# Optimization experiments

Measured on AMD Instinct MI355X. Metric: run time of the kernel, lower is better.

Reference implementation:

```python
import jax, jax.numpy as jnp
import numpy as np
import math

D = 256   # d_model / hidden_size
Q = 256   # q_num (query-side nodes)
K = 512   # k_num (key-side nodes)
NEG = -9e15


def _forward(q_enc, k_enc, rel_k, rel_v, k_adj,
             W_glob, b_glob, W_gv0, b_gv0, W_gv1, b_gv1,
             W_gq, b_gq, W_lq, b_lq,
             W_locgate, b_locgate, W_gate, b_gate):
    d = q_enc.shape[-1]
    scale = 1.0 / math.sqrt(d)
    act = jnp.tanh  # activation_func='tanh'

    # --- global sigmoid blending of k_enc with the mean query encoding ---
    q_glob_enc = jnp.mean(q_enc, axis=0)                       # [d]
    k_s = jax.nn.sigmoid((q_glob_enc @ W_glob + b_glob) @ k_enc.T * scale)  # [K]
    k_s = k_s[:, None]                                         # [K,1]
    g_1 = q_glob_enc @ W_gv0 + b_gv0                           # [d]
    k_1 = k_enc @ W_gv1 + b_gv1                                # [K,d]
    k_enc2 = (1.0 - k_s) * k_1 + k_s * g_1                     # [K,d]

    # --- global relation-aware attention over k nodes ---
    q_glob = q_enc @ W_gq + b_gq                               # [Q,d]
    qk_logit = q_glob @ k_enc2.T                               # [Q,K]
    qk_r = jnp.einsum('qd,qkd->qk', q_glob, rel_k)             # [Q,K]
    glob_attn = jax.nn.softmax(act((qk_logit + qk_r) * scale), axis=-1)  # [Q,K]

    # --- local adjacency-masked attention ---
    q_loc = q_enc @ W_lq + b_lq                                # [Q,d]
    qnk_logit = q_loc @ k_enc2.T                               # [Q,K]
    qnk_r = jnp.einsum('qd,qkd->qk', q_loc, rel_k)             # [Q,K]
    loc_attn = act((qnk_logit + qnk_r) * scale)                # [Q,K]
    # loc_weight_rep[q,i,j] = loc_attn[q,j]  (repeat + view in torch)
    mask = (k_adj != 0)[None, :, :]                            # [1,K,K]
    masked = jnp.where(mask, loc_attn[:, None, :], NEG)        # [Q,K,K]
    attn_adj_norm = jax.nn.softmax(masked, axis=-1)            # [Q,K,K]
    k_loc = jnp.einsum('qij,jd->qid', attn_adj_norm, k_enc2)   # [Q,K,d]

    # --- local gate between neighborhood value and self value ---
    # sigmoid(cat([k_loc, k_self]) @ W_locgate + b); k_self is broadcast k_enc2
    Wg1, Wg2 = W_locgate[:d], W_locgate[d:]                    # [d,1] each
    gate_logit = (jnp.einsum('qid,d->qi', k_loc, Wg1[:, 0])
                  + (k_enc2 @ Wg2)[None, :, 0] + b_locgate[0])  # [Q,K]
    loc_gate = jax.nn.sigmoid(gate_logit)[..., None]           # [Q,K,1]
    k_awr = loc_gate * k_loc + (1.0 - loc_gate) * k_enc2[None, :, :]  # [Q,K,d]

    # --- aggregate with global attention + relation values ---
    k_matmul = jnp.einsum('qk,qkd->qd', glob_attn, k_awr)      # [Q,d]
    k_r_matmul = jnp.einsum('qk,qkd->qd', glob_attn, rel_v)    # [Q,d]
    q_enc_new = k_matmul + k_r_matmul                          # [Q,d]

    # --- residual gate ---
    Wq1, Wq2 = W_gate[:d], W_gate[d:]
    gate = jax.nn.sigmoid(q_enc_new @ Wq1 + q_enc @ Wq2 + b_gate)  # [Q,1]
    h = gate * q_enc_new + (1.0 - gate) * q_enc                # [Q,d]
    return h


def setup_inputs() -> dict:
    key = jax.random.key(0)
    ks = jax.random.split(key, 16)
    def w(k, shape):
        return jax.random.normal(k, shape, jnp.float32) * 0.02
    return {
        'q_enc': jax.random.normal(ks[0], (Q, D), jnp.float32),
        'k_enc': jax.random.normal(ks[1], (K, D), jnp.float32),
        'rel_k': jax.random.normal(ks[2], (Q, K, D), jnp.float32) * 0.1,
        'rel_v': jax.random.normal(ks[3], (Q, K, D), jnp.float32) * 0.1,
        'k_adj': jax.random.randint(ks[4], (K, K), 0, 2, jnp.int64) if jax.config.jax_enable_x64 else jax.random.randint(ks[4], (K, K), 0, 2, jnp.int32),
        'W_glob': w(ks[5], (D, D)), 'b_glob': jnp.zeros((D,), jnp.float32),
        'W_gv0': w(ks[6], (D, D)), 'b_gv0': jnp.zeros((D,), jnp.float32),
        'W_gv1': w(ks[7], (D, D)), 'b_gv1': jnp.zeros((D,), jnp.float32),
        'W_gq': w(ks[8], (D, D)), 'b_gq': jnp.zeros((D,), jnp.float32),
        'W_lq': w(ks[9], (D, D)), 'b_lq': jnp.zeros((D,), jnp.float32),
        'W_locgate': w(ks[10], (2 * D, 1)), 'b_locgate': jnp.zeros((1,), jnp.float32),
        'W_gate': w(ks[11], (2 * D, 1)), 'b_gate': jnp.zeros((1,), jnp.float32),
    }


def reference(q_enc, k_enc, rel_k, rel_v, k_adj,
              W_glob, b_glob, W_gv0, b_gv0, W_gv1, b_gv1,
              W_gq, b_gq, W_lq, b_lq,
              W_locgate, b_locgate, W_gate, b_gate):
    return _forward(q_enc, k_enc, rel_k, rel_v, k_adj,
                    W_glob, b_glob, W_gv0, b_gv0, W_gv1, b_gv1,
                    W_gq, b_gq, W_lq, b_lq,
                    W_locgate, b_locgate, W_gate, b_gate)
```

## Files before the change

kernel.cpp:

```cpp
#include <hip/hip_runtime.h>
#include <math.h>

#define QN 256
#define KN 512
#define DN 256
#define SCALE 0.0625f

typedef __attribute__((ext_vector_type(8))) short short8v;
typedef __attribute__((ext_vector_type(4))) float f32x4;

__device__ __forceinline__ float sigf(float x){ return 1.0f/(1.0f+expf(-x)); }

__device__ __forceinline__ unsigned short f2bf(float x){
  unsigned u = __float_as_uint(x);
  unsigned r = (u + 0x7FFFu + ((u >> 16) & 1u)) >> 16;
  return (unsigned short)r;
}

__device__ __forceinline__ float bfdec(unsigned v){
  return __uint_as_float(v << 16);
}

__device__ __forceinline__ short8v ld8(const unsigned short* p){
  ushort4 a = *(const ushort4*)p;
  ushort4 b = *(const ushort4*)(p + 16);
  short8v r;
  r[0]=(short)a.x; r[1]=(short)a.y; r[2]=(short)a.z; r[3]=(short)a.w;
  r[4]=(short)b.x; r[5]=(short)b.y; r[6]=(short)b.z; r[7]=(short)b.w;
  return r;
}

__device__ __forceinline__ float wave_red(float v){
  #pragma unroll
  for (int off = 32; off; off >>= 1) v += __shfl_down(v, off);
  return v;
}

__global__ void kA2(const float* __restrict__ q_enc,
                    const float* __restrict__ W_glob, const float* __restrict__ W_gv0,
                    float* __restrict__ party0, float* __restrict__ party1,
                    const int* __restrict__ kadj, unsigned short* __restrict__ mbf){
  __shared__ float sm[256][9];
  __shared__ float qm[8];
  int b = blockIdx.x, t = threadIdx.x;
  int j0 = b*8;
  #pragma unroll
  for (int i = 0; i < 8; ++i){
    int gi = b*2048 + i*256 + t;
    int4 v = ((const int4*)kadj)[gi];
    ushort4 o;
    o.x = v.x ? 0x3F80 : 0; o.y = v.y ? 0x3F80 : 0;
    o.z = v.z ? 0x3F80 : 0; o.w = v.w ? 0x3F80 : 0;
    ((ushort4*)mbf)[gi] = o;
  }
  float4 lo = *(const float4*)(q_enc + (size_t)t*DN + j0);
  float4 hi = *(const float4*)(q_enc + (size_t)t*DN + j0 + 4);
  sm[t][0]=lo.x; sm[t][1]=lo.y; sm[t][2]=lo.z; sm[t][3]=lo.w;
  sm[t][4]=hi.x; sm[t][5]=hi.y; sm[t][6]=hi.z; sm[t][7]=hi.w;
  __syncthreads();
  #pragma unroll
  for (int s = 128; s > 0; s >>= 1){
    if (t < s){
      #pragma unroll
      for (int j = 0; j < 8; ++j) sm[t][j] += sm[t+s][j];
    }
    __syncthreads();
  }
  if (t < 8) qm[t] = sm[0][t] * (1.0f/QN);
  __syncthreads();
  float a0 = 0.f, a1 = 0.f;
  #pragma unroll
  for (int j = 0; j < 8; ++j){
    float s = qm[j];
    a0 = fmaf(s, W_glob[(size_t)(j0+j)*DN + t], a0);
    a1 = fmaf(s, W_gv0[(size_t)(j0+j)*DN + t], a1);
  }
  party0[b*256 + t] = a0; party1[b*256 + t] = a1;
}

__global__ void k23(const float* __restrict__ k_enc,
                    const float* __restrict__ W_gv1, const float* __restrict__ b_gv1,
                    const float* __restrict__ party0, const float* __restrict__ party1,
                    const float* __restrict__ b_glob, const float* __restrict__ b_gv0,
                    const float* __restrict__ W_locgate,
                    float* __restrict__ k_enc2, float* __restrict__ cvec,
                    float* __restrict__ gl2,
                    const float* __restrict__ q_enc,
                    const float* __restrict__ W_gq, const float* __restrict__ b_gq,
                    const float* __restrict__ W_lq, const float* __restrict__ b_lq,
                    float* __restrict__ q_glob, float* __restrict__ q_loc){
  __shared__ float sh1[256];
  __shared__ float red8[8];
  int bid = blockIdx.x, t = threadIdx.x;
  int w = t >> 6, lane = t & 63;
  if (bid < 512){
    int k = bid;
    float tg = b_glob[t], g1v = b_gv0[t];
    #pragma unroll 8
    for (int b2 = 0; b2 < 32; ++b2){
      tg  += party0[b2*256 + t];
      g1v += party1[b2*256 + t];
    }
    float kv = k_enc[(size_t)k*DN + t];
    sh1[t] = kv;
    float part = wave_red(kv * tg);
    if (lane == 0) red8[w] = part;
    __syncthreads();
    float dot = red8[0] + red8[1] + red8[2] + red8[3];
    float ks = sigf(dot * SCALE);
    float acc = b_gv1[t];
    #pragma unroll 8
    for (int j = 0; j < DN; ++j) acc = fmaf(sh1[j], W_gv1[(size_t)j*DN + t], acc);
    float v = (1.f - ks)*acc + ks*g1v;
    k_enc2[(size_t)k*DN + t] = v;
    float pc = wave_red(v * W_locgate[t]);
    float pg = wave_red(v * W_locgate[DN + t]);
    __syncthreads();
    if (lane == 0){ red8[w] = pc; red8[4 + w] = pg; }
    __syncthreads();
    if (t == 0) cvec[k] = red8[0] + red8[1] + red8[2] + red8[3];
    if (t == 1) gl2[k]  = red8[4] + red8[5] + red8[6] + red8[7];
  } else {
    int q = bid - 512;
    sh1[t] = q_enc[(size_t)q*DN + t];
    __syncthreads();
    float a = b_gq[t], b = b_lq[t];
    #pragma unroll 8
    for (int j = 0; j < DN; ++j){
      float s = sh1[j];
      a = fmaf(s, W_gq[(size_t)j*DN + t], a);
      b = fmaf(s, W_lq[(size_t)j*DN + t], b);
    }
    q_glob[(size_t)q*DN + t] = a; q_loc[(size_t)q*DN + t] = b;
  }
}

__global__ __launch_bounds__(256) void kbf(const float* __restrict__ rel_k,
                    const float* __restrict__ rel_v,
                    const float* __restrict__ q_glob, const float* __restrict__ q_loc,
                    const float* __restrict__ ke2, const float* __restrict__ cvec,
                    float* __restrict__ exs,
                    unsigned short* __restrict__ ebf, unsigned short* __restrict__ ecbf,
                    float* __restrict__ part){
  __shared__ unsigned short y_lds[32*264];
  __shared__ float2 p_lds[32];
  __shared__ float  ex_s[32];
  __shared__ f32x4  pacc[4][64];
  int t = threadIdx.x;
  int wv = t >> 6, lane = t & 63;
  int g = lane >> 4, l16 = lane & 15;
  int b = blockIdx.x;
  int q = b >> 4, slice = b & 15;
  float4 a4[4], b4[4];
  #pragma unroll
  for (int it = 0; it < 4; ++it){
    int d = it*64 + l16*4;
    a4[it] = *(const float4*)(q_glob + (size_t)q*DN + d);
    b4[it] = *(const float4*)(q_loc  + (size_t)q*DN + d);
  }
  #pragma unroll
  for (int kq = 0; kq < 2; ++kq){
    int kl = kq*16 + wv*4 + g;
    int k  = slice*32 + kl;
    size_t ro = ((size_t)q*KN + k)*DN;
    float p13 = 0.f, p24 = 0.f;
    #pragma unroll
    for (int it = 0; it < 4; ++it){
      int d = it*64 + l16*4;
      f32x4 x = *(const f32x4*)(rel_k + ro + d);
      f32x4 y = *(const f32x4*)(rel_v + ro + d);
      float4 c = *(const float4*)(ke2 + (size_t)k*DN + d);
      float4 a = a4[it], bb = b4[it];
      p13 += (x[0]+c.x)*a.x  + (x[1]+c.y)*a.y  + (x[2]+c.z)*a.z  + (x[3]+c.w)*a.w;
      p24 += (x[0]+c.x)*bb.x + (x[1]+c.y)*bb.y + (x[2]+c.z)*bb.z + (x[3]+c.w)*bb.w;
      unsigned lo, hi;
      asm("v_cvt_pk_bf16_f32 %0, %1, %2" : "=v"(lo) : "v"(y[0]), "v"(y[1]));
      asm("v_cvt_pk_bf16_f32 %0, %1, %2" : "=v"(hi) : "v"(y[2]), "v"(y[3]));
      *(uint2*)&y_lds[kl*264 + d] = make_uint2(lo, hi);
    }
    #pragma unroll
    for (int off = 8; off; off >>= 1){
      p13 += __shfl_down(p13, off);
      p24 += __shfl_down(p24, off);
    }
    if (l16 == 0) p_lds[kl] = make_float2(p13, p24);
  }
  __syncthreads();
  if (t < 32){
    int k = slice*32 + t;
    float2 p = p_lds[t];
    float exv = expf(tanhf(p.x*SCALE));
    float evv = expf(tanhf(p.y*SCALE));
    size_t idx = (size_t)q*KN + k;
    exs[idx] = exv;
    ebf[idx] = f2bf(evv);
    ecbf[idx] = f2bf(evv * cvec[k]);
    ex_s[t] = exv;
  }
  __syncthreads();
  {
    int chunk = t & 63, quarter = t >> 6;
    f32x4 r = {0.f, 0.f, 0.f, 0.f};
    #pragma unroll
    for (int i = 0; i < 8; ++i){
      int kk = quarter*8 + i;
      uint2 yy = *(const uint2*)&y_lds[kk*264 + chunk*4];
      float e = ex_s[kk];
      r[0] = fmaf(e, bfdec(yy.x & 0xFFFFu), r[0]);
      r[1] = fmaf(e, bfdec(yy.x >> 16),     r[1]);
      r[2] = fmaf(e, bfdec(yy.y & 0xFFFFu), r[2]);
      r[3] = fmaf(e, bfdec(yy.y >> 16),     r[3]);
    }
    pacc[quarter][chunk] = r;
  }
  __syncthreads();
  if (t < 64){
    f32x4 r = pacc[0][t];
    f32x4 r1 = pacc[1][t], r2 = pacc[2][t], r3 = pacc[3][t];
    r[0] += r1[0] + r2[0] + r3[0];
    r[1] += r1[1] + r2[1] + r3[1];
    r[2] += r1[2] + r2[2] + r3[2];
    r[3] += r1[3] + r2[3] + r3[3];
    *(f32x4*)(part + ((size_t)slice*QN + q)*DN + t*4) = r;
  }
}

__global__ __launch_bounds__(256) void kcA2m(const unsigned short* __restrict__ ebf,
                                             const unsigned short* __restrict__ ecbf,
                                             const unsigned short* __restrict__ mbf,
                                             const float* __restrict__ exs,
                                             const float* __restrict__ gl2,
                                             const float* __restrict__ blg_p,
                                             unsigned short* __restrict__ wvbf,
                                             float* __restrict__ v2){
  __shared__ unsigned short Ae[16*520];
  __shared__ unsigned short Ac[16*520];
  __shared__ unsigned short Bm[64*520];
  int t = threadIdx.x;
  int i0 = blockIdx.x*64, q0 = blockIdx.y*16;
  #pragma unroll
  for (int it = 0; it < 4; ++it){
    int c = t + 256*it; int row = c >> 6, col = (c & 63)*8;
    *(uint4*)&Ae[row*520 + col] = *(const uint4*)&ebf[(size_t)(q0+row)*KN + col];
    *(uint4*)&Ac[row*520 + col] = *(const uint4*)&ecbf[(size_t)(q0+row)*KN + col];
  }
  #pragma unroll
  for (int it = 0; it < 16; ++it){
    int c = t + 256*it; int row = c >> 6, col = (c & 63)*8;
    *(uint4*)&Bm[row*520 + col] = *(const uint4*)&mbf[(size_t)(i0+row)*KN + col];
  }
  __syncthreads();
  int w = t >> 6, l = t & 63;
  int g16 = l >> 4, l16 = l & 15;
  f32x4 aS = {0.f,0.f,0.f,0.f}, aN = {0.f,0.f,0.f,0.f};
  const unsigned short* pe = &Ae[l16*520];
  const unsigned short* pc = &Ac[l16*520];
  const unsigned short* pb = &Bm[(16*w + l16)*520];
  #pragma unroll
  for (int kk = 0; kk < 16; ++kk){
    int k0 = kk*32 + 4*g16;
    short8v fa = ld8(pe + k0);
    short8v fc = ld8(pc + k0);
    short8v fb = ld8(pb + k0);
    aS = __builtin_amdgcn_mfma_f32_16x16x32_bf16(fa, fb, aS, 0, 0, 0);
    aN = __builtin_amdgcn_mfma_f32_16x16x32_bf16(fc, fb, aN, 0, 0, 0);
  }
  float blg = blg_p[0];
  int i = i0 + 16*w + l16;
  float gli = gl2[i];
  #pragma unroll
  for (int r = 0; r < 4; ++r){
    int q = q0 + 4*g16 + r;
    size_t idx = (size_t)q*KN + i;
    float s = aS[r], n = aN[r];
    float lgv = sigf(n/s + gli + blg);
    float ex = exs[idx];
    wvbf[idx] = f2bf(ex*lgv/s);
    v2[idx] = ex*(1.f - lgv);
  }
}

__global__ __launch_bounds__(1024) void kE3(const float* __restrict__ ke2,
                                            const float* __restrict__ exs,
                                            const unsigned short* __restrict__ wvbf,
                                            const unsigned short* __restrict__ mbf,
                                            const unsigned short* __restrict__ ebf,
                                            const float* __restrict__ v2,
                                            const float* __restrict__ part,
                                            const float* __restrict__ q_enc,
                                            const float* __restrict__ W_gate,
                                            const float* __restrict__ b_gate,
                                            float* __restrict__ out){
  __shared__ float red[512];
  __shared__ float wvs[512];
  __shared__ float sacc[4][512];
  __shared__ float coefs[512];
  __shared__ float4 pacc[16][64];
  int q = blockIdx.x, t = threadIdx.x, w = t >> 6, lane = t & 63;
  if (t < 512){
    red[t] = exs[(size_t)q*KN + t];
    wvs[t] = __uint_as_float(((unsigned)wvbf[(size_t)q*KN + t]) << 16);
  }
  __syncthreads();
  #pragma unroll
  for (int s = 256; s > 0; s >>= 1){
    if (t < s) red[t] += red[t+s];
    __syncthreads();
  }
  float invs = 1.0f / red[0];
  {
    int tq = t & 255, ti = t >> 8;
    int j0 = tq*2;
    float a0 = 0.f, a1 = 0.f;
    int ibase = ti*128;
    #pragma unroll 8
    for (int ii = 0; ii < 128; ++ii){
      int i = ibase + ii;
      unsigned mm = *(const unsigned*)(mbf + (size_t)i*KN + j0);
      float wvi = wvs[i];
      a0 = fmaf(wvi, __uint_as_float((mm & 0xFFFFu) << 16), a0);
      a1 = fmaf(wvi, __uint_as_float((mm >> 16) << 16), a1);
    }
    sacc[ti][j0] = a0; sacc[ti][j0+1] = a1;
  }
  __syncthreads();
  if (t < 512){
    float u = sacc[0][t] + sacc[1][t] + sacc[2][t] + sacc[3][t];
    float evv = __uint_as_float(((unsigned)ebf[(size_t)q*KN + t]) << 16);
    coefs[t] = u*evv + v2[(size_t)q*KN + t];
  }
  __syncthreads();
  f32x4 pv = *(const f32x4*)(part + ((size_t)w*QN + q)*DN + lane*4);
  float4 acc = make_float4(pv[0], pv[1], pv[2], pv[3]);
  int kbase = w*32;
  #pragma unroll 8
  for (int kk = 0; kk < 32; ++kk){
    int k = kbase + kk;
    float ck = coefs[k];
    float4 kv = ((const float4*)(ke2 + (size_t)k*DN))[lane];
    acc.x = fmaf(ck, kv.x, acc.x);
    acc.y = fmaf(ck, kv.y, acc.y);
    acc.z = fmaf(ck, kv.z, acc.z);
    acc.w = fmaf(ck, kv.w, acc.w);
  }
  pacc[w][lane] = acc;
  __syncthreads();
  if (t < 64){
    float4 r = pacc[0][t];
    #pragma unroll
    for (int w2 = 1; w2 < 16; ++w2){
      float4 p = pacc[w2][t];
      r.x += p.x; r.y += p.y; r.z += p.z; r.w += p.w;
    }
    r.x *= invs; r.y *= invs; r.z *= invs; r.w *= invs;
    float4 qe = ((const float4*)(q_enc + (size_t)q*DN))[t];
    float4 w1 = ((const float4*)(W_gate))[t];
    float4 w2v = ((const float4*)(W_gate + DN))[t];
    float pd = r.x*w1.x + r.y*w1.y + r.z*w1.z + r.w*w1.w
             + qe.x*w2v.x + qe.y*w2v.y + qe.z*w2v.z + qe.w*w2v.w;
    #pragma unroll
    for (int off = 32; off; off >>= 1) pd += __shfl_down(pd, off);
    float gate = sigf(__shfl(pd, 0) + b_gate[0]);
    float4 h;
    h.x = gate*r.x + (1.f-gate)*qe.x;
    h.y = gate*r.y + (1.f-gate)*qe.y;
    h.z = gate*r.z + (1.f-gate)*qe.z;
    h.w = gate*r.w + (1.f-gate)*qe.w;
    ((float4*)(out + (size_t)q*DN))[t] = h;
  }
}

extern "C" void kernel_launch(void* const* d_in, const int* in_sizes, int n_in,
                              void* d_out, int out_size, void* d_ws, size_t ws_size,
                              hipStream_t stream){
  const float* q_enc     = (const float*)d_in[0];
  const float* k_enc     = (const float*)d_in[1];
  const float* rel_k     = (const float*)d_in[2];
  const float* rel_v     = (const float*)d_in[3];
  const int*   k_adj     = (const int*)  d_in[4];
  const float* W_glob    = (const float*)d_in[5];
  const float* b_glob    = (const float*)d_in[6];
  const float* W_gv0     = (const float*)d_in[7];
  const float* b_gv0     = (const float*)d_in[8];
  const float* W_gv1     = (const float*)d_in[9];
  const float* b_gv1     = (const float*)d_in[10];
  const float* W_gq      = (const float*)d_in[11];
  const float* b_gq      = (const float*)d_in[12];
  const float* W_lq      = (const float*)d_in[13];
  const float* b_lq      = (const float*)d_in[14];
  const float* W_locgate = (const float*)d_in[15];
  const float* b_locgate = (const float*)d_in[16];
  const float* W_gate    = (const float*)d_in[17];
  const float* b_gate    = (const float*)d_in[18];
  float* out = (float*)d_out;

  float* ws = (float*)d_ws;
  float* party0   = ws;
  float* party1   = party0 + 8192;
  float* k_enc2   = party1 + 8192;
  float* cvec     = k_enc2 + 131072;
  float* gl2      = cvec + 512;
  float* q_glob   = gl2 + 512;
  float* q_loc    = q_glob + 65536;
  float* exs      = q_loc + 65536;
  float* v2       = exs + 131072;
  float* part     = v2 + 131072;
  unsigned short* mbf  = (unsigned short*)(part + 1048576);
  unsigned short* ebf  = mbf + 262144;
  unsigned short* ecbf = ebf + 131072;
  unsigned short* wvbf = ecbf + 131072;

  kA2<<<32, 256, 0, stream>>>(q_enc, W_glob, W_gv0, party0, party1, k_adj, mbf);
  k23<<<768, 256, 0, stream>>>(k_enc, W_gv1, b_gv1, party0, party1, b_glob, b_gv0,
                               W_locgate, k_enc2, cvec, gl2,
                               q_enc, W_gq, b_gq, W_lq, b_lq, q_glob, q_loc);
  kbf<<<4096, 256, 0, stream>>>(rel_k, rel_v, q_glob, q_loc, k_enc2, cvec,
                                exs, ebf, ecbf, part);
  kcA2m<<<dim3(8, 16), 256, 0, stream>>>(ebf, ecbf, mbf, exs, gl2, b_locgate, wvbf, v2);
  kE3<<<256, 1024, 0, stream>>>(k_enc2, exs, wvbf, mbf, ebf, v2, part,
                                q_enc, W_gate, b_gate, out);
}
```

Measured before the change: 86.36 us.

## Split q·k_enc2 logits into separate tiled GEMM kernel before relation pass

Moves the q_glob/q_loc dot products with k_enc2 out of the streaming rel_k kernel into a new LDS-tiled GEMM kernel that writes the paired logits to workspace. The bandwidth-bound kbf kernel then reads only rel_k and rel_v plus one float2 per (q,k), instead of re-reading k_enc2 rows for every query. This costs an extra kernel launch and a 2 MB intermediate write and read.

```diff
diff --git a/kernel.cpp b/kernel.cpp
--- a/kernel.cpp
+++ b/kernel.cpp
@@ -135,10 +135,56 @@
   }
 }
 
+__global__ __launch_bounds__(128) void kP(const float* __restrict__ qg,
+                                          const float* __restrict__ ql,
+                                          const float* __restrict__ ke2,
+                                          float2* __restrict__ p34){
+  __shared__ float sA[64][18], sL[64][18], sB[64][34];
+  int t = threadIdx.x;
+  int q0 = blockIdx.y*16, k0 = blockIdx.x*32;
+  int tq = t & 7, tk = t >> 3;
+  float a1[2][2] = {{0.f,0.f},{0.f,0.f}}, a2[2][2] = {{0.f,0.f},{0.f,0.f}};
+  for (int d0 = 0; d0 < DN; d0 += 64){
+    #pragma unroll
+    for (int r = 0; r < 2; ++r){
+      int f = t + 128*r; int row = f >> 4; int c4 = (f & 15)*4;
+      float4 va = *(const float4*)(qg + (size_t)(q0+row)*DN + d0 + c4);
+      float4 vl = *(const float4*)(ql + (size_t)(q0+row)*DN + d0 + c4);
+      sA[c4+0][row]=va.x; sA[c4+1][row]=va.y; sA[c4+2][row]=va.z; sA[c4+3][row]=va.w;
+      sL[c4+0][row]=vl.x; sL[c4+1][row]=vl.y; sL[c4+2][row]=vl.z; sL[c4+3][row]=vl.w;
+    }
+    #pragma unroll
+    for (int r = 0; r < 4; ++r){
+      int f = t + 128*r; int row = f >> 4; int c4 = (f & 15)*4;
+      float4 vb = *(const float4*)(ke2 + (size_t)(k0+row)*DN + d0 + c4);
+      sB[c4+0][row]=vb.x; sB[c4+1][row]=vb.y; sB[c4+2][row]=vb.z; sB[c4+3][row]=vb.w;
+    }
+    __syncthreads();
+    #pragma unroll 8
+    for (int d = 0; d < 64; ++d){
+      float2 av = *(const float2*)&sA[d][tq*2];
+      float2 lv = *(const float2*)&sL[d][tq*2];
+      float2 bv = *(const float2*)&sB[d][tk*2];
+      a1[0][0] = fmaf(av.x, bv.x, a1[0][0]); a1[0][1] = fmaf(av.x, bv.y, a1[0][1]);
+      a1[1][0] = fmaf(av.y, bv.x, a1[1][0]); a1[1][1] = fmaf(av.y, bv.y, a1[1][1]);
+      a2[0][0] = fmaf(lv.x, bv.x, a2[0][0]); a2[0][1] = fmaf(lv.x, bv.y, a2[0][1]);
+      a2[1][0] = fmaf(lv.y, bv.x, a2[1][0]); a2[1][1] = fmaf(lv.y, bv.y, a2[1][1]);
+    }
+    __syncthreads();
+  }
+  #pragma unroll
+  for (int qq = 0; qq < 2; ++qq)
+    #pragma unroll
+    for (int kk = 0; kk < 2; ++kk){
+      int q = q0 + tq*2 + qq, k = k0 + tk*2 + kk;
+      p34[(size_t)q*KN + k] = make_float2(a1[qq][kk], a2[qq][kk]);
+    }
+}
+
 __global__ __launch_bounds__(256) void kbf(const float* __restrict__ rel_k,
                     const float* __restrict__ rel_v,
                     const float* __restrict__ q_glob, const float* __restrict__ q_loc,
-                    const float* __restrict__ ke2, const float* __restrict__ cvec,
+                    const float2* __restrict__ p34, const float* __restrict__ cvec,
                     float* __restrict__ exs,
                     unsigned short* __restrict__ ebf, unsigned short* __restrict__ ecbf,
                     float* __restrict__ part){
@@ -169,10 +215,9 @@
       int d = it*64 + l16*4;
       f32x4 x = *(const f32x4*)(rel_k + ro + d);
       f32x4 y = *(const f32x4*)(rel_v + ro + d);
-      float4 c = *(const float4*)(ke2 + (size_t)k*DN + d);
       float4 a = a4[it], bb = b4[it];
-      p13 += (x[0]+c.x)*a.x  + (x[1]+c.y)*a.y  + (x[2]+c.z)*a.z  + (x[3]+c.w)*a.w;
-      p24 += (x[0]+c.x)*bb.x + (x[1]+c.y)*bb.y + (x[2]+c.z)*bb.z + (x[3]+c.w)*bb.w;
+      p13 += x[0]*a.x  + x[1]*a.y  + x[2]*a.z  + x[3]*a.w;
+      p24 += x[0]*bb.x + x[1]*bb.y + x[2]*bb.z + x[3]*bb.w;
       unsigned lo, hi;
       asm("v_cvt_pk_bf16_f32 %0, %1, %2" : "=v"(lo) : "v"(y[0]), "v"(y[1]));
       asm("v_cvt_pk_bf16_f32 %0, %1, %2" : "=v"(hi) : "v"(y[2]), "v"(y[3]));
@@ -189,9 +234,10 @@
   if (t < 32){
     int k = slice*32 + t;
     float2 p = p_lds[t];
-    float exv = expf(tanhf(p.x*SCALE));
-    float evv = expf(tanhf(p.y*SCALE));
     size_t idx = (size_t)q*KN + k;
+    float2 pv = p34[idx];
+    float exv = expf(tanhf((p.x + pv.x)*SCALE));
+    float evv = expf(tanhf((p.y + pv.y)*SCALE));
     exs[idx] = exv;
     ebf[idx] = f2bf(evv);
     ecbf[idx] = f2bf(evv * cvec[k]);
@@ -405,16 +451,19 @@
   float* exs      = q_loc + 65536;
   float* v2       = exs + 131072;
   float* part     = v2 + 131072;
-  unsigned short* mbf  = (unsigned short*)(part + 1048576);
+  float* p34f     = part + 1048576;
+  unsigned short* mbf  = (unsigned short*)(p34f + 262144);
   unsigned short* ebf  = mbf + 262144;
   unsigned short* ecbf = ebf + 131072;
   unsigned short* wvbf = ecbf + 131072;
+  float2* p34 = (float2*)p34f;
 
   kA2<<<32, 256, 0, stream>>>(q_enc, W_glob, W_gv0, party0, party1, k_adj, mbf);
   k23<<<768, 256, 0, stream>>>(k_enc, W_gv1, b_gv1, party0, party1, b_glob, b_gv0,
                                W_locgate, k_enc2, cvec, gl2,
                                q_enc, W_gq, b_gq, W_lq, b_lq, q_glob, q_loc);
-  kbf<<<4096, 256, 0, stream>>>(rel_k, rel_v, q_glob, q_loc, k_enc2, cvec,
+  kP<<<dim3(16, 16), 128, 0, stream>>>(q_glob, q_loc, k_enc2, p34);
+  kbf<<<4096, 256, 0, stream>>>(rel_k, rel_v, q_glob, q_loc, p34, cvec,
                                 exs, ebf, ecbf, part);
   kcA2m<<<dim3(8, 16), 256, 0, stream>>>(ebf, ecbf, mbf, exs, gl2, b_locgate, wvbf, v2);
   kE3<<<256, 1024, 0, stream>>>(k_enc2, exs, wvbf, mbf, ebf, v2, part,
```

After: 100.2 us. +16.0%, slower.
